# Optimization experiments

Measured on AMD Instinct MI355X. Metric: run time of the kernel, lower is better.

## Reference

```python
import jax, jax.numpy as jnp
import numpy as np

TOP_K = 2

def setup_inputs() -> dict:
    key = jax.random.key(0)
    kx, kg, k1, k2 = jax.random.split(key, 4)
    B, T, D, E, H = 4, 1024, 1024, 8, 2048
    x = jax.random.normal(kx, (B, T, D), dtype=jnp.float32)
    Wg = jax.random.normal(kg, (D, E), dtype=jnp.float32) * 0.02
    W1 = jax.random.normal(k1, (E, D, H), dtype=jnp.float32) * 0.02  # c_fc per expert
    W2 = jax.random.normal(k2, (E, H, D), dtype=jnp.float32) * 0.02  # c_proj per expert
    return {"x": x, "Wg": Wg, "W1": W1, "W2": W2}

def reference(x, Wg, W1, W2):
    B, T, D = x.shape
    E = W1.shape[0]
    # Router: softmax over experts, top-k, renormalize top-k weights
    logits = jnp.einsum('btd,de->bte', x, Wg)          # (B,T,E)
    probs = jax.nn.softmax(logits, axis=-1)
    top_w, top_i = jax.lax.top_k(probs, TOP_K)          # (B,T,K)
    top_w = top_w / (jnp.sum(top_w, axis=-1, keepdims=True) + 1e-8)
    # Combine weights per (token, expert): sum_k top_w[k] * one_hot(top_i[k])
    N = B * T
    oh = jax.nn.one_hot(top_i.reshape(N, TOP_K), E, dtype=x.dtype)   # (N,K,E)
    combine = jnp.sum(oh * top_w.reshape(N, TOP_K)[..., None], axis=1)  # (N,E)
    # Expert MLPs: relu(x W1)^2 W2, evaluated densely and combined (same math)
    xt = x.reshape(N, D)
    h = jnp.einsum('td,edh->teh', xt, W1)               # (N,E,H)
    h = jnp.square(jax.nn.relu(h))
    y = jnp.einsum('teh,ehd->ted', h, W2)               # (N,E,D)
    out = jnp.einsum('te,ted->td', combine, y)          # (N,D)
    return out.reshape(B, T, D)
```

## Files before the change

### kernel.cpp

```cpp
#include <hip/hip_runtime.h>
#include <hip/hip_bf16.h>
#include <stdint.h>

#define NTOK 4096
#define DD 1024
#define EE 8
#define HH 2048
#define BM 128
#define BN 128
#define BK 64
#define MAXRB 72
#define RPAD (MAXRB*BM)
#define GG1 (8*9*(HH/BN))
#define GG2 (8*9*(DD/BN))

typedef __attribute__((ext_vector_type(4))) float f32x4;
typedef __attribute__((ext_vector_type(8))) short bf16x8;

__device__ __forceinline__ void gload16(const void* g, void* l) {
  __builtin_amdgcn_global_load_lds((const __attribute__((address_space(1))) unsigned int*)g,
                                   (__attribute__((address_space(3))) unsigned int*)l, 16, 0, 0);
}

__device__ __forceinline__ void transpose_body(uint32_t (*T)[33],
    const float* __restrict__ in, __hip_bfloat16* __restrict__ out,
    int R, int C, int tb) {
  int tilesC = C >> 6;
  int tilesPerE = (R >> 6) * tilesC;
  int e = tb / tilesPerE;
  int rem = tb % tilesPerE;
  int tr = rem / tilesC, tc = rem % tilesC;
  const float* src = in + (size_t)e * R * C + (size_t)(tr*64) * C + tc*64;
  int tid = threadIdx.x;
  int c0  = (tid & 31) * 2;
  int r2b = tid >> 5;
  #pragma unroll
  for (int i = 0; i < 4; ++i) {
    int r2 = r2b + 8*i;
    const float* p0 = src + (size_t)(2*r2) * C + c0;
    float2 a = *(const float2*)p0;
    float2 b = *(const float2*)(p0 + C);
    uint32_t u0 = ((uint32_t)__bfloat16_as_ushort(__float2bfloat16(b.x)) << 16)
                |  (uint32_t)__bfloat16_as_ushort(__float2bfloat16(a.x));
    uint32_t u1 = ((uint32_t)__bfloat16_as_ushort(__float2bfloat16(b.y)) << 16)
                |  (uint32_t)__bfloat16_as_ushort(__float2bfloat16(a.y));
    T[c0][r2]   = u0;
    T[c0+1][r2] = u1;
  }
  __syncthreads();
  __hip_bfloat16* dst = out + (size_t)e * R * C + (size_t)(tc*64) * R + tr*64;
  int c  = tid >> 2;
  int ch = (tid & 3) * 8;
  uint32_t v[8];
  #pragma unroll
  for (int j = 0; j < 8; ++j) v[j] = T[c][ch + j];
  uint32_t* dp = (uint32_t*)(dst + (size_t)c * R + ch*2);
  #pragma unroll
  for (int j = 0; j < 8; ++j) dp[j] = v[j];
}

__global__ __launch_bounds__(256) void mega_kernel(const float* __restrict__ x,
    const float* __restrict__ Wg, double* __restrict__ logitsD,
    const float* __restrict__ W1, __hip_bfloat16* __restrict__ W1bT) {
  __shared__ __align__(16) char smem[8448];
  int b = blockIdx.x;
  if (b < NTOK) {
    int t = b;
    int tid = threadIdx.x;
    const float* xr = x + (size_t)t * DD;
    double acc[EE];
    #pragma unroll
    for (int e = 0; e < EE; ++e) acc[e] = 0.0;
    #pragma unroll
    for (int i = 0; i < DD/256; ++i) {
      int d = tid + i*256;
      float xv = xr[d];
      float4 w0 = *(const float4*)(Wg + (size_t)d*EE);
      float4 w1 = *(const float4*)(Wg + (size_t)d*EE + 4);
      double xd = (double)xv;
      acc[0] += xd * (double)w0.x; acc[1] += xd * (double)w0.y;
      acc[2] += xd * (double)w0.z; acc[3] += xd * (double)w0.w;
      acc[4] += xd * (double)w1.x; acc[5] += xd * (double)w1.y;
      acc[6] += xd * (double)w1.z; acc[7] += xd * (double)w1.w;
    }
    #pragma unroll
    for (int e = 0; e < EE; ++e) {
      double v = acc[e];
      #pragma unroll
      for (int off = 32; off > 0; off >>= 1) v += __shfl_down(v, off, 64);
      acc[e] = v;
    }
    double (*sAcc)[EE] = (double(*)[EE])smem;
    int lane = tid & 63, w = tid >> 6;
    if (lane == 0) {
      #pragma unroll
      for (int e = 0; e < EE; ++e) sAcc[w][e] = acc[e];
    }
    __syncthreads();
    if (tid < EE)
      logitsD[(size_t)t*EE + tid] = sAcc[0][tid] + sAcc[1][tid] + sAcc[2][tid] + sAcc[3][tid];
  } else {
    transpose_body((uint32_t(*)[33])smem, W1, W1bT, DD, HH, b - NTOK);
  }
}

__global__ __launch_bounds__(256) void softtop_kernel(const double* __restrict__ logitsD,
    int* __restrict__ topE, float* __restrict__ topW, int* __restrict__ counts) {
  __shared__ int hist[EE];
  if (threadIdx.x < EE) hist[threadIdx.x] = 0;
  __syncthreads();
  int t = blockIdx.x * 256 + threadIdx.x;
  double s[EE];
  #pragma unroll
  for (int e = 0; e < EE; ++e) s[e] = logitsD[(size_t)t*EE + e];
  double mx = s[0];
  #pragma unroll
  for (int e = 1; e < EE; ++e) mx = fmax(mx, s[e]);
  double p[EE], Z = 0.0;
  #pragma unroll
  for (int e = 0; e < EE; ++e) { p[e] = exp(s[e] - mx); Z += p[e]; }
  #pragma unroll
  for (int e = 0; e < EE; ++e) p[e] /= Z;
  int i0 = 0;
  #pragma unroll
  for (int e = 1; e < EE; ++e) if (p[e] > p[i0]) i0 = e;
  int i1 = -1;
  #pragma unroll
  for (int e = 0; e < EE; ++e) { if (e == i0) continue; if (i1 < 0 || p[e] > p[i1]) i1 = e; }
  double sm = p[i0] + p[i1] + 1e-8;
  topE[t*2]   = i0; topE[t*2+1] = i1;
  topW[t*2]   = (float)(p[i0] / sm);
  topW[t*2+1] = (float)(p[i1] / sm);
  atomicAdd(&hist[i0], 1); atomicAdd(&hist[i1], 1);
  __syncthreads();
  if (threadIdx.x < EE) atomicAdd(&counts[threadIdx.x], hist[threadIdx.x]);
}

__global__ __launch_bounds__(1024) void assign_kernel(const int* __restrict__ counts,
    const int* __restrict__ topE, const float* __restrict__ topW,
    int* __restrict__ po, int* __restrict__ nRB, int* __restrict__ rbExpert,
    int* __restrict__ pairsTok, float* __restrict__ pairsW, int* __restrict__ slotOf) {
  __shared__ int base[EE];
  __shared__ int wcnt[16][EE];
  int tid = threadIdx.x, wv = tid >> 6, lane = tid & 63;
  if (tid == 0) {
    int off = 0;
    for (int e = 0; e < EE; ++e) {
      po[e] = off;
      off += ((counts[e] + BM - 1) / BM) * BM;
    }
    po[EE] = off;
    *nRB = off / BM;
    int rb = 0;
    for (int e = 0; e < EE; ++e) {
      int nb = (counts[e] + BM - 1) / BM;
      for (int b = 0; b < nb; ++b) rbExpert[rb++] = e;
    }
  }
  for (int i = tid; i < RPAD; i += 1024) pairsTok[i] = -1;
  __syncthreads();
  if (tid < EE) base[tid] = po[tid];
  __syncthreads();
  for (int it = 0; it < 2*NTOK/1024; ++it) {
    int p = it*1024 + tid;
    int e = topE[p];
    int myrank = 0;
    #pragma unroll
    for (int ee = 0; ee < EE; ++ee) {
      unsigned long long b = __ballot(e == ee);
      if (ee == e) myrank = __popcll(b & ((1ull << lane) - 1ull));
      if (lane == 0) wcnt[wv][ee] = __popcll(b);
    }
    __syncthreads();
    int wbase = 0;
    for (int w2 = 0; w2 < wv; ++w2) wbase += wcnt[w2][e];
    int slot = base[e] + wbase + myrank;
    pairsTok[slot] = p >> 1;
    pairsW[slot]   = topW[p];
    slotOf[p]      = slot;
    __syncthreads();
    if (tid < EE) {
      int s2 = 0;
      #pragma unroll
      for (int w2 = 0; w2 < 16; ++w2) s2 += wcnt[w2][tid];
      base[tid] += s2;
    }
    __syncthreads();
  }
}

__global__ __launch_bounds__(256) void gather_kernel(const float* __restrict__ x,
    const int* __restrict__ slotOf, __hip_bfloat16* __restrict__ Xg) {
  int t = blockIdx.x;
  int s0 = slotOf[2*t], s1 = slotOf[2*t+1];
  const float* xr = x + (size_t)t * DD;
  int i = threadIdx.x;
  float4 v = ((const float4*)xr)[i];
  ushort4 b;
  b.x = __bfloat16_as_ushort(__float2bfloat16(v.x));
  b.y = __bfloat16_as_ushort(__float2bfloat16(v.y));
  b.z = __bfloat16_as_ushort(__float2bfloat16(v.z));
  b.w = __bfloat16_as_ushort(__float2bfloat16(v.w));
  ((ushort4*)(Xg + (size_t)s0 * DD))[i] = b;
  ((ushort4*)(Xg + (size_t)s1 * DD))[i] = b;
}

template<int EPI, int KDIM, int NTOT>
__device__ __forceinline__ void gemm_body(char* smem, int bid,
    const __hip_bfloat16* __restrict__ A, const __hip_bfloat16* __restrict__ Ball,
    __hip_bfloat16* __restrict__ Cbf, float* __restrict__ Cf,
    const int* __restrict__ nRB, const int* __restrict__ rbExpert,
    const int* __restrict__ pairsTok, const float* __restrict__ pairsW) {
  int nrb = *nRB;
  int cpx = (nrb + 7) >> 3;
  int xcd = bid & 7;
  int slot = bid >> 3;
  int lr = slot % 9;
  int nb = slot / 9;
  int rb = xcd * cpx + lr;
  if (lr >= cpx || rb >= nrb) return;
  int e = rbExpert[rb];
  const __hip_bfloat16* Ag = A + (size_t)rb * BM * KDIM;
  const __hip_bfloat16* Bg = Ball + (size_t)e * NTOT * KDIM + (size_t)nb * BN * KDIM;
  __hip_bfloat16* As = (__hip_bfloat16*)smem;
  __hip_bfloat16* Bs = (__hip_bfloat16*)(smem + 16384);
  int*   sTok = (int*)(smem + 32768);
  float* sW   = (float*)(smem + 32768 + 512);
  int tid = threadIdx.x;
  if (EPI == 1 && tid < BM) {
    sTok[tid] = pairsTok[rb*BM + tid];
    sW[tid]   = pairsW[rb*BM + tid];
  }
  int lane = tid & 63;
  int wid = tid >> 6;
  int wr = wid >> 1, wc = wid & 1;
  int l15 = lane & 15;
  int lhi = lane >> 4;
  f32x4 acc[4][4] = {};
  int srow  = tid >> 3;
  int scol8 = (tid & 7) * 8;
  for (int kt = 0; kt < KDIM / BK; ++kt) {
    #pragma unroll
    for (int i = 0; i < 4; ++i) {
      int r = srow + 32*i;
      int sc = scol8 ^ ((r & 7) << 3);
      gload16(Ag + (size_t)r * KDIM + kt*BK + sc, (char*)As + i*4096 + tid*16);
      gload16(Bg + (size_t)r * KDIM + kt*BK + sc, (char*)Bs + i*4096 + tid*16);
    }
    __syncthreads();
    #pragma unroll
    for (int kk = 0; kk < 2; ++kk) {
      bf16x8 af[4], bfr[4];
      int kb = kk*64 + lhi*16;
      #pragma unroll
      for (int m = 0; m < 4; ++m) {
        int row = wr*64 + m*16 + l15;
        af[m] = *(const bf16x8*)((const char*)As + row*128 + (kb ^ ((row & 7) << 4)));
      }
      #pragma unroll
      for (int n = 0; n < 4; ++n) {
        int row = wc*64 + n*16 + l15;
        bfr[n] = *(const bf16x8*)((const char*)Bs + row*128 + (kb ^ ((row & 7) << 4)));
      }
      #pragma unroll
      for (int m = 0; m < 4; ++m)
        #pragma unroll
        for (int n = 0; n < 4; ++n)
          acc[m][n] = __builtin_amdgcn_mfma_f32_16x16x32_bf16(af[m], bfr[n], acc[m][n], 0, 0, 0);
    }
    __syncthreads();
  }
  if (EPI == 0) {
    #pragma unroll
    for (int m = 0; m < 4; ++m) {
      int row = rb*BM + wr*64 + m*16 + lhi*4;
      #pragma unroll
      for (int n = 0; n < 4; ++n) {
        int col = nb*BN + wc*64 + n*16 + l15;
        #pragma unroll
        for (int j = 0; j < 4; ++j) {
          float v = fmaxf(acc[m][n][j], 0.0f);
          Cbf[(size_t)(row + j) * NTOT + col] = __float2bfloat16(v * v);
        }
      }
    }
  } else {
    #pragma unroll
    for (int m = 0; m < 4; ++m) {
      int rloc = wr*64 + m*16 + lhi*4;
      #pragma unroll
      for (int j = 0; j < 4; ++j) {
        int tok = sTok[rloc + j];
        if (tok < 0) continue;
        float w = sW[rloc + j];
        #pragma unroll
        for (int n = 0; n < 4; ++n) {
          int col = nb*BN + wc*64 + n*16 + l15;
          atomicAdd(Cf + (size_t)tok * NTOT + col, w * acc[m][n][j]);
        }
      }
    }
  }
}

__global__ __launch_bounds__(256, 4)
void gemm1_fused(const __hip_bfloat16* __restrict__ Xg,
                 const __hip_bfloat16* __restrict__ W1bT,
                 __hip_bfloat16* __restrict__ Hbuf,
                 const int* __restrict__ nRB, const int* __restrict__ rbExpert,
                 const int* __restrict__ pairsTok, const float* __restrict__ pairsW,
                 const float* __restrict__ W2, __hip_bfloat16* __restrict__ W2bT) {
  __shared__ __align__(16) char smem[33*1024 + 1024];
  int bid = blockIdx.x;
  if (bid < GG1) {
    gemm_body<0, DD, HH>(smem, bid, Xg, W1bT, Hbuf, nullptr,
                         nRB, rbExpert, pairsTok, pairsW);
  } else {
    transpose_body((uint32_t(*)[33])smem, W2, W2bT, HH, DD, bid - GG1);
  }
}

__global__ __launch_bounds__(256, 4)
void gemm2_kernel(const __hip_bfloat16* __restrict__ Hbuf,
                  const __hip_bfloat16* __restrict__ W2bT,
                  float* __restrict__ out,
                  const int* __restrict__ nRB, const int* __restrict__ rbExpert,
                  const int* __restrict__ pairsTok, const float* __restrict__ pairsW) {
  __shared__ __align__(16) char smem[33*1024 + 1024];
  gemm_body<1, HH, DD>(smem, blockIdx.x, Hbuf, W2bT, nullptr, out,
                       nRB, rbExpert, pairsTok, pairsW);
}


extern "C" void kernel_launch(void* const* d_in, const int* in_sizes, int n_in,
                              void* d_out, int out_size, void* d_ws, size_t ws_size,
                              hipStream_t stream) {
  const float* x  = (const float*)d_in[0];
  const float* Wg = (const float*)d_in[1];
  const float* W1 = (const float*)d_in[2];
  const float* W2 = (const float*)d_in[3];
  float* out = (float*)d_out;
  char* ws = (char*)d_ws;

  int*   counts   = (int*)(ws + 0);
  int*   po       = (int*)(ws + 128);
  int*   nRB      = (int*)(ws + 192);
  int*   rbExpert = (int*)(ws + 256);
  int*   topE     = (int*)(ws + 1024);
  float* topW     = (float*)(ws + 40960);
  int*   pairsTok = (int*)(ws + 73728);
  float* pairsW   = (float*)(ws + 110592);
  int*   slotOf   = (int*)(ws + 147456);
  __hip_bfloat16* Xg   = (__hip_bfloat16*)(ws + 262144);
  __hip_bfloat16* Hbuf = (__hip_bfloat16*)(ws + 19136512);
  double* logitsD = (double*)(ws + 19136512);
  __hip_bfloat16* W1bT = (__hip_bfloat16*)(ws + 56885248);
  __hip_bfloat16* W2bT = (__hip_bfloat16*)(ws + 90439680);

  hipMemsetAsync(d_out, 0, (size_t)out_size * sizeof(float), stream);
  hipMemsetAsync(ws, 0, 128, stream);

  mega_kernel<<<NTOK + 4096, 256, 0, stream>>>(x, Wg, logitsD, W1, W1bT);
  softtop_kernel<<<NTOK/256, 256, 0, stream>>>(logitsD, topE, topW, counts);
  assign_kernel<<<1, 1024, 0, stream>>>(counts, topE, topW, po, nRB, rbExpert,
                                        pairsTok, pairsW, slotOf);
  gather_kernel<<<NTOK, 256, 0, stream>>>(x, slotOf, Xg);

  gemm1_fused<<<GG1 + 4096, 256, 0, stream>>>(Xg, W1bT, Hbuf, nRB, rbExpert,
                                              pairsTok, pairsW, W2, W2bT);
  gemm2_kernel<<<GG2, 256, 0, stream>>>(Hbuf, W2bT, out, nRB, rbExpert,
                                        pairsTok, pairsW);
}
```

Before: 195.1 us.

## Fuse both expert GEMMs into one launch with per-row-block readiness flags

Moves the W2 transpose into the first mega kernel and merges GEMM1 and GEMM2 into a single launch. GEMM2 blocks spin on a per-row-block counter until all 16 GEMM1 column tiles for that row block are done, so the second GEMM can overlap the tail of the first. It also reorders GEMM1 tile mapping so column tiles of a row block sit in adjacent slots. The intent is to remove the kernel boundary and launch gap between the GEMMs. The cost is spin-waiting blocks that occupy CUs, and a deadlock risk if GEMM2 blocks get scheduled ahead of the GEMM1 blocks they wait on.

```diff
diff --git a/kernel.cpp b/kernel.cpp
--- a/kernel.cpp
+++ b/kernel.cpp
@@ -61,7 +61,8 @@
 
 __global__ __launch_bounds__(256) void mega_kernel(const float* __restrict__ x,
     const float* __restrict__ Wg, double* __restrict__ logitsD,
-    const float* __restrict__ W1, __hip_bfloat16* __restrict__ W1bT) {
+    const float* __restrict__ W1, __hip_bfloat16* __restrict__ W1bT,
+    const float* __restrict__ W2, __hip_bfloat16* __restrict__ W2bT) {
   __shared__ __align__(16) char smem[8448];
   int b = blockIdx.x;
   if (b < NTOK) {
@@ -99,8 +100,10 @@
     __syncthreads();
     if (tid < EE)
       logitsD[(size_t)t*EE + tid] = sAcc[0][tid] + sAcc[1][tid] + sAcc[2][tid] + sAcc[3][tid];
+  } else if (b < NTOK + 4096) {
+    transpose_body((uint32_t(*)[33])smem, W1, W1bT, DD, HH, b - NTOK);
   } else {
-    transpose_body((uint32_t(*)[33])smem, W1, W1bT, DD, HH, b - NTOK);
+    transpose_body((uint32_t(*)[33])smem, W2, W2bT, HH, DD, b - NTOK - 4096);
   }
 }
 
@@ -206,19 +209,11 @@
 }
 
 template<int EPI, int KDIM, int NTOT>
-__device__ __forceinline__ void gemm_body(char* smem, int bid,
+__device__ __forceinline__ void gemm_body(char* smem, int rb, int nb,
     const __hip_bfloat16* __restrict__ A, const __hip_bfloat16* __restrict__ Ball,
     __hip_bfloat16* __restrict__ Cbf, float* __restrict__ Cf,
-    const int* __restrict__ nRB, const int* __restrict__ rbExpert,
+    const int* __restrict__ rbExpert,
     const int* __restrict__ pairsTok, const float* __restrict__ pairsW) {
-  int nrb = *nRB;
-  int cpx = (nrb + 7) >> 3;
-  int xcd = bid & 7;
-  int slot = bid >> 3;
-  int lr = slot % 9;
-  int nb = slot / 9;
-  int rb = xcd * cpx + lr;
-  if (lr >= cpx || rb >= nrb) return;
   int e = rbExpert[rb];
   const __hip_bfloat16* Ag = A + (size_t)rb * BM * KDIM;
   const __hip_bfloat16* Bg = Ball + (size_t)e * NTOT * KDIM + (size_t)nb * BN * KDIM;
@@ -304,31 +299,45 @@
 }
 
 __global__ __launch_bounds__(256, 4)
-void gemm1_fused(const __hip_bfloat16* __restrict__ Xg,
-                 const __hip_bfloat16* __restrict__ W1bT,
-                 __hip_bfloat16* __restrict__ Hbuf,
-                 const int* __restrict__ nRB, const int* __restrict__ rbExpert,
-                 const int* __restrict__ pairsTok, const float* __restrict__ pairsW,
-                 const float* __restrict__ W2, __hip_bfloat16* __restrict__ W2bT) {
+void gemm_fused(const __hip_bfloat16* __restrict__ Xg,
+                const __hip_bfloat16* __restrict__ W1bT,
+                __hip_bfloat16* __restrict__ Hbuf,
+                const __hip_bfloat16* __restrict__ W2bT,
+                float* __restrict__ out,
+                const int* __restrict__ nRB, const int* __restrict__ rbExpert,
+                const int* __restrict__ pairsTok, const float* __restrict__ pairsW,
+                int* __restrict__ hflag) {
   __shared__ __align__(16) char smem[33*1024 + 1024];
+  int nrb = *nRB;
+  int cpx = (nrb + 7) >> 3;
   int bid = blockIdx.x;
   if (bid < GG1) {
-    gemm_body<0, DD, HH>(smem, bid, Xg, W1bT, Hbuf, nullptr,
-                         nRB, rbExpert, pairsTok, pairsW);
+    int xcd = bid & 7, slot = bid >> 3;
+    int nb = slot & 15, lr = slot >> 4;
+    int rb = xcd * cpx + lr;
+    if (lr >= cpx || rb >= nrb) return;
+    gemm_body<0, DD, HH>(smem, rb, nb, Xg, W1bT, Hbuf, nullptr,
+                         rbExpert, pairsTok, pairsW);
+    __syncthreads();
+    if (threadIdx.x == 0)
+      __hip_atomic_fetch_add(&hflag[rb*16], 1, __ATOMIC_RELEASE,
+                             __HIP_MEMORY_SCOPE_AGENT);
   } else {
-    transpose_body((uint32_t(*)[33])smem, W2, W2bT, HH, DD, bid - GG1);
-  }
-}
-
-__global__ __launch_bounds__(256, 4)
-void gemm2_kernel(const __hip_bfloat16* __restrict__ Hbuf,
-                  const __hip_bfloat16* __restrict__ W2bT,
-                  float* __restrict__ out,
-                  const int* __restrict__ nRB, const int* __restrict__ rbExpert,
-                  const int* __restrict__ pairsTok, const float* __restrict__ pairsW) {
-  __shared__ __align__(16) char smem[33*1024 + 1024];
-  gemm_body<1, HH, DD>(smem, blockIdx.x, Hbuf, W2bT, nullptr, out,
-                       nRB, rbExpert, pairsTok, pairsW);
+    int b2 = bid - GG1;
+    int xcd = b2 & 7, slot = b2 >> 3;
+    int lr = slot % 9, nb = slot / 9;
+    int rb = xcd * cpx + lr;
+    if (lr >= cpx || rb >= nrb) return;
+    if (threadIdx.x == 0) {
+      while (__hip_atomic_load(&hflag[rb*16], __ATOMIC_RELAXED,
+                               __HIP_MEMORY_SCOPE_AGENT) < 16)
+        __builtin_amdgcn_s_sleep(16);
+      __builtin_amdgcn_fence(__ATOMIC_ACQUIRE, "agent");
+    }
+    __syncthreads();
+    gemm_body<1, HH, DD>(smem, rb, nb, Hbuf, W2bT, nullptr, out,
+                         rbExpert, pairsTok, pairsW);
+  }
 }
 
 
@@ -351,6 +360,7 @@
   int*   pairsTok = (int*)(ws + 73728);
   float* pairsW   = (float*)(ws + 110592);
   int*   slotOf   = (int*)(ws + 147456);
+  int*   hflag    = (int*)(ws + 180224);
   __hip_bfloat16* Xg   = (__hip_bfloat16*)(ws + 262144);
   __hip_bfloat16* Hbuf = (__hip_bfloat16*)(ws + 19136512);
   double* logitsD = (double*)(ws + 19136512);
@@ -359,15 +369,14 @@
 
   hipMemsetAsync(d_out, 0, (size_t)out_size * sizeof(float), stream);
   hipMemsetAsync(ws, 0, 128, stream);
-
-  mega_kernel<<<NTOK + 4096, 256, 0, stream>>>(x, Wg, logitsD, W1, W1bT);
+  hipMemsetAsync(ws + 180224, 0, 4608, stream);
+
+  mega_kernel<<<NTOK + 8192, 256, 0, stream>>>(x, Wg, logitsD, W1, W1bT, W2, W2bT);
   softtop_kernel<<<NTOK/256, 256, 0, stream>>>(logitsD, topE, topW, counts);
   assign_kernel<<<1, 1024, 0, stream>>>(counts, topE, topW, po, nRB, rbExpert,
                                         pairsTok, pairsW, slotOf);
   gather_kernel<<<NTOK, 256, 0, stream>>>(x, slotOf, Xg);
 
-  gemm1_fused<<<GG1 + 4096, 256, 0, stream>>>(Xg, W1bT, Hbuf, nRB, rbExpert,
-                                              pairsTok, pairsW, W2, W2bT);
-  gemm2_kernel<<<GG2, 256, 0, stream>>>(Hbuf, W2bT, out, nRB, rbExpert,
-                                        pairsTok, pairsW);
-}
+  gemm_fused<<<GG1 + GG2, 256, 0, stream>>>(Xg, W1bT, Hbuf, W2bT, out,
+                                            nRB, rbExpert, pairsTok, pairsW, hflag);
+}
```

Result: slower. 236.8 us (+21.4%).

## Fuse softmax/top-k routing into router kernel and widen transpose loads

Applied to the files above, without the earlier changes.

Moves the softmax, top-2 selection and weight normalisation into the router blocks of the mega kernel, removing the separate softtop kernel launch and the double-precision logits round trip through global memory. Expert counts are spread over 64 slots to reduce atomic contention, and assign_kernel sums those slots. The W1 transpose now uses float4 loads instead of float2. This saves one launch and some memory traffic, at the cost of serial work on thread 0 in each router block and more global atomics.

```diff
diff --git a/kernel.cpp b/kernel.cpp
--- a/kernel.cpp
+++ b/kernel.cpp
@@ -22,6 +22,11 @@
                                    (__attribute__((address_space(3))) unsigned int*)l, 16, 0, 0);
 }
 
+__device__ __forceinline__ uint32_t pack_bf2(float lo, float hi) {
+  return ((uint32_t)__bfloat16_as_ushort(__float2bfloat16(hi)) << 16)
+       |  (uint32_t)__bfloat16_as_ushort(__float2bfloat16(lo));
+}
+
 __device__ __forceinline__ void transpose_body(uint32_t (*T)[33],
     const float* __restrict__ in, __hip_bfloat16* __restrict__ out,
     int R, int C, int tb) {
@@ -32,20 +37,18 @@
   int tr = rem / tilesC, tc = rem % tilesC;
   const float* src = in + (size_t)e * R * C + (size_t)(tr*64) * C + tc*64;
   int tid = threadIdx.x;
-  int c0  = (tid & 31) * 2;
-  int r2b = tid >> 5;
+  int c4 = (tid & 15) << 2;
+  int r2 = tid >> 4;
   #pragma unroll
-  for (int i = 0; i < 4; ++i) {
-    int r2 = r2b + 8*i;
-    const float* p0 = src + (size_t)(2*r2) * C + c0;
-    float2 a = *(const float2*)p0;
-    float2 b = *(const float2*)(p0 + C);
-    uint32_t u0 = ((uint32_t)__bfloat16_as_ushort(__float2bfloat16(b.x)) << 16)
-                |  (uint32_t)__bfloat16_as_ushort(__float2bfloat16(a.x));
-    uint32_t u1 = ((uint32_t)__bfloat16_as_ushort(__float2bfloat16(b.y)) << 16)
-                |  (uint32_t)__bfloat16_as_ushort(__float2bfloat16(a.y));
-    T[c0][r2]   = u0;
-    T[c0+1][r2] = u1;
+  for (int i = 0; i < 2; ++i) {
+    int r = r2 + (i << 4);
+    const float* p0 = src + (size_t)(2*r) * C + c4;
+    float4 a = *(const float4*)p0;
+    float4 b = *(const float4*)(p0 + C);
+    T[c4+0][r] = pack_bf2(a.x, b.x);
+    T[c4+1][r] = pack_bf2(a.y, b.y);
+    T[c4+2][r] = pack_bf2(a.z, b.z);
+    T[c4+3][r] = pack_bf2(a.w, b.w);
   }
   __syncthreads();
   __hip_bfloat16* dst = out + (size_t)e * R * C + (size_t)(tc*64) * R + tr*64;
@@ -60,7 +63,8 @@
 }
 
 __global__ __launch_bounds__(256) void mega_kernel(const float* __restrict__ x,
-    const float* __restrict__ Wg, double* __restrict__ logitsD,
+    const float* __restrict__ Wg,
+    int* __restrict__ topE, float* __restrict__ topW, int* __restrict__ counts64,
     const float* __restrict__ W1, __hip_bfloat16* __restrict__ W1bT) {
   __shared__ __align__(16) char smem[8448];
   int b = blockIdx.x;
@@ -97,67 +101,68 @@
       for (int e = 0; e < EE; ++e) sAcc[w][e] = acc[e];
     }
     __syncthreads();
-    if (tid < EE)
-      logitsD[(size_t)t*EE + tid] = sAcc[0][tid] + sAcc[1][tid] + sAcc[2][tid] + sAcc[3][tid];
+    if (tid == 0) {
+      double s[EE];
+      #pragma unroll
+      for (int e = 0; e < EE; ++e)
+        s[e] = sAcc[0][e] + sAcc[1][e] + sAcc[2][e] + sAcc[3][e];
+      double mx = s[0];
+      #pragma unroll
+      for (int e = 1; e < EE; ++e) mx = fmax(mx, s[e]);
+      double p[EE], Z = 0.0;
+      #pragma unroll
+      for (int e = 0; e < EE; ++e) { p[e] = exp(s[e] - mx); Z += p[e]; }
+      #pragma unroll
+      for (int e = 0; e < EE; ++e) p[e] /= Z;
+      int i0 = 0;
+      #pragma unroll
+      for (int e = 1; e < EE; ++e) if (p[e] > p[i0]) i0 = e;
+      int i1 = -1;
+      #pragma unroll
+      for (int e = 0; e < EE; ++e) { if (e == i0) continue; if (i1 < 0 || p[e] > p[i1]) i1 = e; }
+      double sm = p[i0] + p[i1] + 1e-8;
+      topE[t*2]   = i0; topE[t*2+1] = i1;
+      topW[t*2]   = (float)(p[i0] / sm);
+      topW[t*2+1] = (float)(p[i1] / sm);
+      int slot = (b & 63) * 16;
+      atomicAdd(&counts64[slot + i0], 1);
+      atomicAdd(&counts64[slot + i1], 1);
+    }
   } else {
     transpose_body((uint32_t(*)[33])smem, W1, W1bT, DD, HH, b - NTOK);
   }
 }
 
-__global__ __launch_bounds__(256) void softtop_kernel(const double* __restrict__ logitsD,
-    int* __restrict__ topE, float* __restrict__ topW, int* __restrict__ counts) {
-  __shared__ int hist[EE];
-  if (threadIdx.x < EE) hist[threadIdx.x] = 0;
-  __syncthreads();
-  int t = blockIdx.x * 256 + threadIdx.x;
-  double s[EE];
-  #pragma unroll
-  for (int e = 0; e < EE; ++e) s[e] = logitsD[(size_t)t*EE + e];
-  double mx = s[0];
-  #pragma unroll
-  for (int e = 1; e < EE; ++e) mx = fmax(mx, s[e]);
-  double p[EE], Z = 0.0;
-  #pragma unroll
-  for (int e = 0; e < EE; ++e) { p[e] = exp(s[e] - mx); Z += p[e]; }
-  #pragma unroll
-  for (int e = 0; e < EE; ++e) p[e] /= Z;
-  int i0 = 0;
-  #pragma unroll
-  for (int e = 1; e < EE; ++e) if (p[e] > p[i0]) i0 = e;
-  int i1 = -1;
-  #pragma unroll
-  for (int e = 0; e < EE; ++e) { if (e == i0) continue; if (i1 < 0 || p[e] > p[i1]) i1 = e; }
-  double sm = p[i0] + p[i1] + 1e-8;
-  topE[t*2]   = i0; topE[t*2+1] = i1;
-  topW[t*2]   = (float)(p[i0] / sm);
-  topW[t*2+1] = (float)(p[i1] / sm);
-  atomicAdd(&hist[i0], 1); atomicAdd(&hist[i1], 1);
-  __syncthreads();
-  if (threadIdx.x < EE) atomicAdd(&counts[threadIdx.x], hist[threadIdx.x]);
-}
-
-__global__ __launch_bounds__(1024) void assign_kernel(const int* __restrict__ counts,
+__global__ __launch_bounds__(1024) void assign_kernel(const int* __restrict__ counts64,
     const int* __restrict__ topE, const float* __restrict__ topW,
     int* __restrict__ po, int* __restrict__ nRB, int* __restrict__ rbExpert,
     int* __restrict__ pairsTok, float* __restrict__ pairsW, int* __restrict__ slotOf) {
+  __shared__ int cnt[EE];
   __shared__ int base[EE];
   __shared__ int wcnt[16][EE];
   int tid = threadIdx.x, wv = tid >> 6, lane = tid & 63;
+  if (tid < EE) {
+    int s = 0;
+    #pragma unroll
+    for (int k = 0; k < 64; ++k) s += counts64[k*16 + tid];
+    cnt[tid] = s;
+  }
+  for (int i = tid; i < RPAD; i += 1024) pairsTok[i] = -1;
+  __syncthreads();
   if (tid == 0) {
     int off = 0;
     for (int e = 0; e < EE; ++e) {
       po[e] = off;
-      off += ((counts[e] + BM - 1) / BM) * BM;
+      off += ((cnt[e] + BM - 1) / BM) * BM;
     }
     po[EE] = off;
     *nRB = off / BM;
     int rb = 0;
     for (int e = 0; e < EE; ++e) {
-      int nb = (counts[e] + BM - 1) / BM;
+      int nb = (cnt[e] + BM - 1) / BM;
       for (int b = 0; b < nb; ++b) rbExpert[rb++] = e;
     }
   }
-  for (int i = tid; i < RPAD; i += 1024) pairsTok[i] = -1;
   __syncthreads();
   if (tid < EE) base[tid] = po[tid];
   __syncthreads();
@@ -342,27 +347,25 @@
   float* out = (float*)d_out;
   char* ws = (char*)d_ws;
 
-  int*   counts   = (int*)(ws + 0);
   int*   po       = (int*)(ws + 128);
   int*   nRB      = (int*)(ws + 192);
   int*   rbExpert = (int*)(ws + 256);
-  int*   topE     = (int*)(ws + 1024);
+  int*   counts64 = (int*)(ws + 4096);
   float* topW     = (float*)(ws + 40960);
   int*   pairsTok = (int*)(ws + 73728);
   float* pairsW   = (float*)(ws + 110592);
   int*   slotOf   = (int*)(ws + 147456);
+  int*   topE     = (int*)(ws + 180224);
   __hip_bfloat16* Xg   = (__hip_bfloat16*)(ws + 262144);
   __hip_bfloat16* Hbuf = (__hip_bfloat16*)(ws + 19136512);
-  double* logitsD = (double*)(ws + 19136512);
   __hip_bfloat16* W1bT = (__hip_bfloat16*)(ws + 56885248);
   __hip_bfloat16* W2bT = (__hip_bfloat16*)(ws + 90439680);
 
   hipMemsetAsync(d_out, 0, (size_t)out_size * sizeof(float), stream);
-  hipMemsetAsync(ws, 0, 128, stream);
-
-  mega_kernel<<<NTOK + 4096, 256, 0, stream>>>(x, Wg, logitsD, W1, W1bT);
-  softtop_kernel<<<NTOK/256, 256, 0, stream>>>(logitsD, topE, topW, counts);
-  assign_kernel<<<1, 1024, 0, stream>>>(counts, topE, topW, po, nRB, rbExpert,
+  hipMemsetAsync(ws, 0, 8192, stream);
+
+  mega_kernel<<<NTOK + 4096, 256, 0, stream>>>(x, Wg, topE, topW, counts64, W1, W1bT);
+  assign_kernel<<<1, 1024, 0, stream>>>(counts64, topE, topW, po, nRB, rbExpert,
                                         pairsTok, pairsW, slotOf);
   gather_kernel<<<NTOK, 256, 0, stream>>>(x, slotOf, Xg);
 
```

After: 192.2 us, median of 2. No clear change (-1.5%).
